# Performance work log

Measured on AMD Instinct MI355X. Metric: run time of the kernel, lower is better.

Reference implementation:

```python
import jax, jax.numpy as jnp
import numpy as np

B, T, F_IN = 256, 168, 128
H = 512            # encoder hidden per direction; decoder hidden = 2H
OUT = 1
L_OUT = 48
SCALE = 0.05


def _lstm_scan(x, Wih, Whh, b, h0, c0):
    # x: [T, B, F]; PyTorch LSTM gate order i, f, g, o
    def step(carry, xt):
        h, c = carry
        g = xt @ Wih.T + h @ Whh.T + b
        i, f, gg, o = jnp.split(g, 4, axis=-1)
        c = jax.nn.sigmoid(f) * c + jax.nn.sigmoid(i) * jnp.tanh(gg)
        h = jax.nn.sigmoid(o) * jnp.tanh(c)
        return (h, c), h
    (hT, cT), ys = jax.lax.scan(step, (h0, c0), x)
    return ys, hT, cT


def setup_inputs() -> dict:
    key = jax.random.key(0)
    ks = jax.random.split(key, 16)
    r = lambda k, shp: (jax.random.normal(k, shp, dtype=jnp.float32) * SCALE)
    return {
        "input_seq": jax.random.normal(ks[0], (B, T, F_IN), dtype=jnp.float32),
        "enc_Wih_f": r(ks[1], (4 * H, F_IN)),
        "enc_Whh_f": r(ks[2], (4 * H, H)),
        "enc_bih_f": r(ks[3], (4 * H,)),
        "enc_bhh_f": r(ks[4], (4 * H,)),
        "enc_Wih_b": r(ks[5], (4 * H, F_IN)),
        "enc_Whh_b": r(ks[6], (4 * H, H)),
        "enc_bih_b": r(ks[7], (4 * H,)),
        "enc_bhh_b": r(ks[8], (4 * H,)),
        "dec_Wih": r(ks[9], (4 * 2 * H, OUT)),
        "dec_Whh": r(ks[10], (4 * 2 * H, 2 * H)),
        "dec_bih": r(ks[11], (4 * 2 * H,)),
        "dec_bhh": r(ks[12], (4 * 2 * H,)),
        "fc_W": r(ks[13], (OUT, 2 * H)),
        "fc_b": r(ks[14], (OUT,)),
        "output_length": L_OUT,
    }


def reference(input_seq, enc_Wih_f, enc_Whh_f, enc_bih_f, enc_bhh_f,
              enc_Wih_b, enc_Whh_b, enc_bih_b, enc_bhh_b,
              dec_Wih, dec_Whh, dec_bih, dec_bhh, fc_W, fc_b, output_length):
    b = input_seq.shape[0]
    h = enc_Whh_f.shape[1]
    x = jnp.transpose(input_seq, (1, 0, 2))  # [T, B, F]
    h0 = jnp.zeros((b, h), input_seq.dtype)
    c0 = jnp.zeros((b, h), input_seq.dtype)
    # bidirectional encoder (final hidden/cell only are used downstream)
    _, hf, cf = _lstm_scan(x, enc_Wih_f, enc_Whh_f, enc_bih_f + enc_bhh_f, h0, c0)
    _, hb, cb = _lstm_scan(x[::-1], enc_Wih_b, enc_Whh_b, enc_bih_b + enc_bhh_b, h0, c0)
    # _cat_hidden: concat fwd/bwd states along feature dim -> decoder init state [B, 2H]
    hd = jnp.concatenate([hf, hb], axis=-1)
    cd = jnp.concatenate([cf, cb], axis=-1)
    bd = dec_bih + dec_bhh
    x0 = jnp.zeros((b, fc_W.shape[0]), input_seq.dtype)  # initial decoder input = zeros

    def dec_step(carry, _):
        hh, cc, xt = carry
        g = xt @ dec_Wih.T + hh @ dec_Whh.T + bd
        i, f, gg, o = jnp.split(g, 4, axis=-1)
        cc = jax.nn.sigmoid(f) * cc + jax.nn.sigmoid(i) * jnp.tanh(gg)
        hh = jax.nn.sigmoid(o) * jnp.tanh(cc)
        pred = hh @ fc_W.T + fc_b  # [B, OUT]
        return (hh, cc, pred), pred

    _, preds = jax.lax.scan(dec_step, (hd, cd, x0), None, length=output_length)
    # [L, B, OUT] -> [B, L, OUT] -> squeeze(dim=2) with OUT==1 -> [B, L]
    return jnp.transpose(preds, (1, 0, 2)).squeeze(2)
```

## Files before the change

kernel.cpp:

```cpp
#include <hip/hip_runtime.h>


constexpr int B_ = 256, T_ = 168, F_ = 128, H_ = 512, L_ = 48;
constexpr int KE = F_ + H_;
constexpr int HD = 1024;
constexpr int GE = 4 * H_;
constexpr int XPAD = 136;
constexpr int DPAD = HD + 8;

constexpr int FL256_IDX  = 0;
constexpr int CLAIM_IDX  = 256;
constexpr int ENCF_IDX   = 768;
constexpr int DECF_IDX   = 2816;
constexpr int CLAIM2_IDX = 3328;
constexpr int FL2_IDX    = 3840;

constexpr size_t OFF_SYNC = 0;
constexpr size_t OFF_WCF = 16384;
constexpr size_t OFF_WCB = OFF_WCF + (size_t)GE * KE * 2;
constexpr size_t OFF_PP  = OFF_WCB + (size_t)GE * KE * 2;
constexpr size_t OFF_BF  = OFF_PP  + (size_t)8 * 2 * 64 * 32 * 4;
constexpr size_t OFF_BB  = OFF_BF  + (size_t)GE * 4;
constexpr size_t OFF_XH  = OFF_BB  + (size_t)GE * 4;
constexpr size_t OFF_HE  = OFF_XH  + (size_t)T_ * B_ * F_ * 2;
constexpr size_t OFF_HDD = OFF_HE  + (size_t)2 * 2 * B_ * H_ * 2;
constexpr size_t OFF_CD  = OFF_HDD + (size_t)2 * B_ * HD * 2;

using h8 = __attribute__((ext_vector_type(8))) _Float16;
using f4 = __attribute__((ext_vector_type(4))) float;
using u4 = __attribute__((ext_vector_type(4))) unsigned;

#define DEV static __device__ __forceinline__

DEV float sigm(float x)  { return __fdividef(1.f, 1.f + __expf(-x)); }
DEV float tanh_(float x) { return 1.f - __fdividef(2.f, __expf(2.f * x) + 1.f); }

DEV h8 as_h8(f4 v) { union { f4 f; h8 h; } u; u.f = v; return u.h; }

DEV void astore_u64(void* p, unsigned long long v) {
  __hip_atomic_store((unsigned long long*)p, v, __ATOMIC_RELAXED,
                     __HIP_MEMORY_SCOPE_AGENT);
}
DEV void astore_u32(void* p, unsigned v) {
  __hip_atomic_store((unsigned*)p, v, __ATOMIC_RELAXED, __HIP_MEMORY_SCOPE_AGENT);
}
DEV unsigned aload_u32(const void* p) {
  return __hip_atomic_load((const unsigned*)p, __ATOMIC_RELAXED,
                           __HIP_MEMORY_SCOPE_AGENT);
}
DEV float aload_f32(const void* p) {
  return __hip_atomic_load((const float*)p, __ATOMIC_RELAXED,
                           __HIP_MEMORY_SCOPE_AGENT);
}
DEV void astore_f32(void* p, float v) {
  __hip_atomic_store((float*)p, v, __ATOMIC_RELAXED, __HIP_MEMORY_SCOPE_AGENT);
}
DEV void astore_u16(void* p, _Float16 v) {
  union { _Float16 h; unsigned short s; } u; u.h = v;
  __hip_atomic_store((unsigned short*)p, u.s, __ATOMIC_RELAXED,
                     __HIP_MEMORY_SCOPE_AGENT);
}
DEV void vm_drain() { asm volatile("s_waitcnt vmcnt(0)" ::: "memory"); }

template<bool DEEP>
DEV void ld16(const _Float16* p, f4* A) {
#define L16(FL) asm volatile( \
    "global_load_dwordx4 %0,  %16, off" FL "\n\t" \
    "global_load_dwordx4 %1,  %16, off offset:64" FL "\n\t" \
    "global_load_dwordx4 %2,  %16, off offset:128" FL "\n\t" \
    "global_load_dwordx4 %3,  %16, off offset:192" FL "\n\t" \
    "global_load_dwordx4 %4,  %16, off offset:256" FL "\n\t" \
    "global_load_dwordx4 %5,  %16, off offset:320" FL "\n\t" \
    "global_load_dwordx4 %6,  %16, off offset:384" FL "\n\t" \
    "global_load_dwordx4 %7,  %16, off offset:448" FL "\n\t" \
    "global_load_dwordx4 %8,  %16, off offset:512" FL "\n\t" \
    "global_load_dwordx4 %9,  %16, off offset:576" FL "\n\t" \
    "global_load_dwordx4 %10, %16, off offset:640" FL "\n\t" \
    "global_load_dwordx4 %11, %16, off offset:704" FL "\n\t" \
    "global_load_dwordx4 %12, %16, off offset:768" FL "\n\t" \
    "global_load_dwordx4 %13, %16, off offset:832" FL "\n\t" \
    "global_load_dwordx4 %14, %16, off offset:896" FL "\n\t" \
    "global_load_dwordx4 %15, %16, off offset:960" FL "\n\t" \
    "s_waitcnt vmcnt(0)" \
    : "=&v"(A[0]),"=&v"(A[1]),"=&v"(A[2]),"=&v"(A[3]),"=&v"(A[4]),"=&v"(A[5]), \
      "=&v"(A[6]),"=&v"(A[7]),"=&v"(A[8]),"=&v"(A[9]),"=&v"(A[10]),"=&v"(A[11]), \
      "=&v"(A[12]),"=&v"(A[13]),"=&v"(A[14]),"=&v"(A[15]) \
    : "v"(p) : "memory")
  if constexpr (DEEP) { L16(" sc0 sc1"); } else { L16(" sc0"); }
#undef L16
}

template<bool DEEP>
DEV void ld32(const _Float16* p, f4* A) {
#define L32(FL) asm volatile( \
    "global_load_dwordx4 %0,  %32, off" FL "\n\t" \
    "global_load_dwordx4 %1,  %32, off offset:64" FL "\n\t" \
    "global_load_dwordx4 %2,  %32, off offset:128" FL "\n\t" \
    "global_load_dwordx4 %3,  %32, off offset:192" FL "\n\t" \
    "global_load_dwordx4 %4,  %32, off offset:256" FL "\n\t" \
    "global_load_dwordx4 %5,  %32, off offset:320" FL "\n\t" \
    "global_load_dwordx4 %6,  %32, off offset:384" FL "\n\t" \
    "global_load_dwordx4 %7,  %32, off offset:448" FL "\n\t" \
    "global_load_dwordx4 %8,  %32, off offset:512" FL "\n\t" \
    "global_load_dwordx4 %9,  %32, off offset:576" FL "\n\t" \
    "global_load_dwordx4 %10, %32, off offset:640" FL "\n\t" \
    "global_load_dwordx4 %11, %32, off offset:704" FL "\n\t" \
    "global_load_dwordx4 %12, %32, off offset:768" FL "\n\t" \
    "global_load_dwordx4 %13, %32, off offset:832" FL "\n\t" \
    "global_load_dwordx4 %14, %32, off offset:896" FL "\n\t" \
    "global_load_dwordx4 %15, %32, off offset:960" FL "\n\t" \
    "global_load_dwordx4 %16, %32, off offset:1024" FL "\n\t" \
    "global_load_dwordx4 %17, %32, off offset:1088" FL "\n\t" \
    "global_load_dwordx4 %18, %32, off offset:1152" FL "\n\t" \
    "global_load_dwordx4 %19, %32, off offset:1216" FL "\n\t" \
    "global_load_dwordx4 %20, %32, off offset:1280" FL "\n\t" \
    "global_load_dwordx4 %21, %32, off offset:1344" FL "\n\t" \
    "global_load_dwordx4 %22, %32, off offset:1408" FL "\n\t" \
    "global_load_dwordx4 %23, %32, off offset:1472" FL "\n\t" \
    "global_load_dwordx4 %24, %32, off offset:1536" FL "\n\t" \
    "global_load_dwordx4 %25, %32, off offset:1600" FL "\n\t" \
    "global_load_dwordx4 %26, %32, off offset:1664" FL "\n\t" \
    "global_load_dwordx4 %27, %32, off offset:1728" FL "\n\t" \
    "global_load_dwordx4 %28, %32, off offset:1792" FL "\n\t" \
    "global_load_dwordx4 %29, %32, off offset:1856" FL "\n\t" \
    "global_load_dwordx4 %30, %32, off offset:1920" FL "\n\t" \
    "global_load_dwordx4 %31, %32, off offset:1984" FL "\n\t" \
    "s_waitcnt vmcnt(0)" \
    : "=&v"(A[0]),"=&v"(A[1]),"=&v"(A[2]),"=&v"(A[3]),"=&v"(A[4]),"=&v"(A[5]), \
      "=&v"(A[6]),"=&v"(A[7]),"=&v"(A[8]),"=&v"(A[9]),"=&v"(A[10]),"=&v"(A[11]), \
      "=&v"(A[12]),"=&v"(A[13]),"=&v"(A[14]),"=&v"(A[15]),"=&v"(A[16]),"=&v"(A[17]), \
      "=&v"(A[18]),"=&v"(A[19]),"=&v"(A[20]),"=&v"(A[21]),"=&v"(A[22]),"=&v"(A[23]), \
      "=&v"(A[24]),"=&v"(A[25]),"=&v"(A[26]),"=&v"(A[27]),"=&v"(A[28]),"=&v"(A[29]), \
      "=&v"(A[30]),"=&v"(A[31]) \
    : "v"(p) : "memory")
  if constexpr (DEEP) { L32(" sc0 sc1"); } else { L32(" sc0"); }
#undef L32
}

DEV void ld32s(const float* p, float* v) {
  asm volatile(
    "global_load_dword %0,  %32, off sc0 sc1\n\t"
    "global_load_dword %1,  %32, off offset:128 sc0 sc1\n\t"
    "global_load_dword %2,  %32, off offset:256 sc0 sc1\n\t"
    "global_load_dword %3,  %32, off offset:384 sc0 sc1\n\t"
    "global_load_dword %4,  %32, off offset:512 sc0 sc1\n\t"
    "global_load_dword %5,  %32, off offset:640 sc0 sc1\n\t"
    "global_load_dword %6,  %32, off offset:768 sc0 sc1\n\t"
    "global_load_dword %7,  %32, off offset:896 sc0 sc1\n\t"
    "global_load_dword %8,  %32, off offset:1024 sc0 sc1\n\t"
    "global_load_dword %9,  %32, off offset:1152 sc0 sc1\n\t"
    "global_load_dword %10, %32, off offset:1280 sc0 sc1\n\t"
    "global_load_dword %11, %32, off offset:1408 sc0 sc1\n\t"
    "global_load_dword %12, %32, off offset:1536 sc0 sc1\n\t"
    "global_load_dword %13, %32, off offset:1664 sc0 sc1\n\t"
    "global_load_dword %14, %32, off offset:1792 sc0 sc1\n\t"
    "global_load_dword %15, %32, off offset:1920 sc0 sc1\n\t"
    "global_load_dword %16, %32, off offset:2048 sc0 sc1\n\t"
    "global_load_dword %17, %32, off offset:2176 sc0 sc1\n\t"
    "global_load_dword %18, %32, off offset:2304 sc0 sc1\n\t"
    "global_load_dword %19, %32, off offset:2432 sc0 sc1\n\t"
    "global_load_dword %20, %32, off offset:2560 sc0 sc1\n\t"
    "global_load_dword %21, %32, off offset:2688 sc0 sc1\n\t"
    "global_load_dword %22, %32, off offset:2816 sc0 sc1\n\t"
    "global_load_dword %23, %32, off offset:2944 sc0 sc1\n\t"
    "global_load_dword %24, %32, off offset:3072 sc0 sc1\n\t"
    "global_load_dword %25, %32, off offset:3200 sc0 sc1\n\t"
    "global_load_dword %26, %32, off offset:3328 sc0 sc1\n\t"
    "global_load_dword %27, %32, off offset:3456 sc0 sc1\n\t"
    "global_load_dword %28, %32, off offset:3584 sc0 sc1\n\t"
    "global_load_dword %29, %32, off offset:3712 sc0 sc1\n\t"
    "global_load_dword %30, %32, off offset:3840 sc0 sc1\n\t"
    "global_load_dword %31, %32, off offset:3968 sc0 sc1\n\t"
    "s_waitcnt vmcnt(0)"
    : "=&v"(v[0]),"=&v"(v[1]),"=&v"(v[2]),"=&v"(v[3]),"=&v"(v[4]),"=&v"(v[5]),
      "=&v"(v[6]),"=&v"(v[7]),"=&v"(v[8]),"=&v"(v[9]),"=&v"(v[10]),"=&v"(v[11]),
      "=&v"(v[12]),"=&v"(v[13]),"=&v"(v[14]),"=&v"(v[15]),"=&v"(v[16]),"=&v"(v[17]),
      "=&v"(v[18]),"=&v"(v[19]),"=&v"(v[20]),"=&v"(v[21]),"=&v"(v[22]),"=&v"(v[23]),
      "=&v"(v[24]),"=&v"(v[25]),"=&v"(v[26]),"=&v"(v[27]),"=&v"(v[28]),"=&v"(v[29]),
      "=&v"(v[30]),"=&v"(v[31])
    : "v"(p) : "memory");
}

DEV unsigned pollflag(const unsigned* p, bool deep) {
  unsigned v;
  if (deep)
    asm volatile("global_load_dword %0, %1, off sc0 sc1\n\t"
                 "s_waitcnt vmcnt(0)" : "=&v"(v) : "v"(p) : "memory");
  else
    asm volatile("global_load_dword %0, %1, off sc0\n\t"
                 "s_waitcnt vmcnt(0)" : "=&v"(v) : "v"(p) : "memory");
  return v;
}
DEV void wait_ge(const unsigned* p, unsigned target, bool deep, int cap) {
  for (int it = 0; it < cap; ++it) {
    unsigned v = pollflag(p, deep);
    if (__ballot(v >= target) == ~0ull) return;
  }
}

DEV void gsync(unsigned* fl, int bi, unsigned phase, int tid) {
  vm_drain();
  __syncthreads();
  if (tid == 0) astore_u32(fl + bi, phase);
  if (tid < 64) {
    const unsigned* p = fl + tid * 4;
    for (int it = 0; it < (1 << 20); ++it) {
      u4 v;
      asm volatile("global_load_dwordx4 %0, %1, off sc0 sc1\n\t"
                   "s_waitcnt vmcnt(0)" : "=&v"(v) : "v"(p) : "memory");
      unsigned a = v[0] < v[1] ? v[0] : v[1];
      unsigned b = v[2] < v[3] ? v[2] : v[3];
      if (__ballot((a < b ? a : b) >= phase) == ~0ull) break;
    }
  }
  __syncthreads();
  asm volatile("" ::: "memory");
}

__global__ void prep_misc(const float* bihF, const float* bhhF,
                          const float* bihB, const float* bhhB, char* ws) {
  int i = blockIdx.x * blockDim.x + threadIdx.x;
  if (i < 2048) astore_u64(ws + (size_t)i * 8, 0ull);
  if (i < GE) {
    ((float*)(ws + OFF_BF))[i] = bihF[i] + bhhF[i];
    ((float*)(ws + OFF_BB))[i] = bihB[i] + bhhB[i];
  }
  if (i < 2 * 2 * B_ * H_ / 4) astore_u64((char*)ws + OFF_HE + (size_t)i * 8, 0ull);
}

__global__ void conv_encw(const float* WihF, const float* WhhF,
                          const float* WihB, const float* WhhB, char* ws) {
  int i = blockIdx.x * blockDim.x + threadIdx.x;
  if (i >= GE * KE) return;
  int r = i / KE, k = i - r * KE;
  float vF = (k < F_) ? WihF[r * F_ + k] : WhhF[r * H_ + (k - F_)];
  float vB = (k < F_) ? WihB[r * F_ + k] : WhhB[r * H_ + (k - F_)];
  ((_Float16*)(ws + OFF_WCF))[i] = (_Float16)vF;
  ((_Float16*)(ws + OFF_WCB))[i] = (_Float16)vB;
}

__global__ void conv_x(const float* x, char* ws) {
  int i = blockIdx.x * blockDim.x + threadIdx.x;
  if (i >= T_ * B_ * F_) return;
  int f = i & 127, b = (i >> 7) & 255, t = i >> 15;
  ((_Float16*)(ws + OFF_XH))[i] = (_Float16)x[((size_t)b * T_ + t) * F_ + f];
}

template<bool LOCAL>
DEV void encoder_phase(int dir, int chunk, int slice,
                       int tid, int wave, int quad, int col, int lane,
                       char* ws, _Float16* xlds, _Float16 (*htile)[64]) {
  const _Float16* Wenc  = (const _Float16*)(ws + (dir ? OFF_WCB : OFF_WCF));
  const float*    biasE = (const float*)(ws + (dir ? OFF_BB : OFF_BF));
  const _Float16* Xh    = (const _Float16*)(ws + OFF_XH);
  _Float16* hE = (_Float16*)(ws + OFF_HE);
  _Float16* hD = (_Float16*)(ws + OFF_HDD);
  float*    cD = (float*)(ws + OFF_CD);
  unsigned* encf = (unsigned*)ws + ENCF_IDX + (dir * 16 + chunk) * 64;

  const int j0 = slice * 64;
  const int mb = chunk * 16;

  for (int it = 0; it < 16; ++it) {
    int idx = it * 256 + tid;
    int n = idx >> 4, e = idx & 15;
    int g = n >> 6, u = n & 63;
    *((h8*)(xlds + (size_t)n * XPAD) + e) =
        *((const h8*)(Wenc + (size_t)(g * H_ + j0 + u) * KE) + e);
  }
  const int unit = j0 + wave * 16 + col;
  h8 Bf[4][16];
#pragma unroll
  for (int g = 0; g < 4; ++g)
#pragma unroll
    for (int kk = 0; kk < 16; ++kk)
      Bf[g][kk] = *((const h8*)(Wenc + (size_t)(g * H_ + unit) * KE + F_) +
                    kk * 4 + quad);
  float breg[4];
#pragma unroll
  for (int g = 0; g < 4; ++g) breg[g] = biasE[g * H_ + unit];
  float cst[4] = {0.f, 0.f, 0.f, 0.f};
  __syncthreads();

  const int arow  = mb + col;
  const int mrowq = mb + quad * 4;

  for (int t = 0; t < T_; ++t) {
    const int par = t & 1;
    const int tx  = dir ? (T_ - 1 - t) : t;
    f4 z = {0.f, 0.f, 0.f, 0.f};
    f4 acc[4] = {z, z, z, z};

    const h8* xr = (const h8*)(Xh + ((size_t)tx * B_ + arow) * F_);
#pragma unroll
    for (int kk = 0; kk < 4; ++kk) {
      h8 a = xr[kk * 4 + quad];
#pragma unroll
      for (int g = 0; g < 4; ++g) {
        h8 b = *((const h8*)(xlds + (size_t)(g * 64 + wave * 16 + col) * XPAD) +
                 kk * 4 + quad);
        acc[g] = __builtin_amdgcn_mfma_f32_16x16x32_f16(a, b, acc[g], 0, 0, 0);
      }
    }
    if (t > 0)
      wait_ge(encf + (lane & 7), (unsigned)t, !LOCAL, 1 << 16);
    f4 A[16];
    ld16<!LOCAL>(hE + ((size_t)(par * 2 + dir) * B_ + arow) * H_ + quad * 8, A);
#pragma unroll
    for (int kk = 0; kk < 16; ++kk) {
      h8 a = as_h8(A[kk]);
#pragma unroll
      for (int g = 0; g < 4; ++g)
        acc[g] = __builtin_amdgcn_mfma_f32_16x16x32_f16(a, Bf[g][kk], acc[g], 0, 0, 0);
    }

#pragma unroll
    for (int r = 0; r < 4; ++r) {
      float gi = acc[0][r] + breg[0];
      float gf = acc[1][r] + breg[1];
      float gg = acc[2][r] + breg[2];
      float go = acc[3][r] + breg[3];
      float c = sigm(gf) * cst[r] + sigm(gi) * tanh_(gg);
      cst[r] = c;
      float h = sigm(go) * tanh_(c);
      htile[quad * 4 + r][wave * 16 + col] = (_Float16)h;
      if (t == T_ - 1)
        astore_f32(&cD[(size_t)(mrowq + r) * HD + dir * H_ + unit], c);
    }
    __syncthreads();
    if (tid < 128) {
      int row = tid >> 3, seg = tid & 7;
      const unsigned long long* src =
          (const unsigned long long*)&htile[row][seg * 8];
      if (t < T_ - 1) {
        _Float16* dst = hE + ((size_t)((par ^ 1) * 2 + dir) * B_ + mb + row) * H_ +
                        j0 + seg * 8;
        if (LOCAL) {
          ((unsigned long long*)dst)[0] = src[0];
          ((unsigned long long*)(dst + 4))[0] = src[1];
        } else {
          astore_u64(dst, src[0]);
          astore_u64(dst + 4, src[1]);
        }
      } else {
        _Float16* dst = hD + (size_t)(mb + row) * HD + dir * H_ + j0 + seg * 8;
        astore_u64(dst, src[0]);
        astore_u64(dst + 4, src[1]);
      }
    }
    vm_drain();
    __syncthreads();
    if (tid == 0 && t < T_ - 1) {
      if (LOCAL) *(volatile unsigned*)(encf + slice) = (unsigned)(t + 1);
      else       astore_u32(encf + slice, (unsigned)(t + 1));
    }
  }
}

DEV void decoder_phase(int xcd, int rank, int tid, int wave, int quad, int col,
                       int lane, const float* dWih, const float* dWhh,
                       const float* dbih, const float* dbhh, const float* fcW,
                       const float* fcb, float* out, char* ws, _Float16* lds,
                       float* predbuf) {
  _Float16* hdd = (_Float16*)(ws + OFF_HDD);
  float* cD = (float*)(ws + OFF_CD);
  float* PP = (float*)(ws + OFF_PP) + (size_t)xcd * 2 * 64 * 32;
  unsigned* decf = (unsigned*)ws + DECF_IDX + xcd * 64;

  const int j0b = rank * 32;
  const int R0  = xcd * 32;
  const int m   = wave & 1;
  const int uh  = wave >> 1;
  const int unit = j0b + uh * 16 + col;
  const int arow = R0 + m * 16 + col;
  const int mrow = R0 + m * 16 + quad * 4;

  for (int it = 0; it < 64; ++it) {
    int idx = it * 256 + tid;
    int n = idx >> 8, c = idx & 255;
    int srow = (n >> 5) * HD + j0b + (n & 31);
    f4 w = *((const f4*)(dWhh + (size_t)srow * HD + c * 4));
    union { _Float16 h[4]; unsigned long long q; } u2;
#pragma unroll
    for (int i2 = 0; i2 < 4; ++i2) u2.h[i2] = (_Float16)w[i2];
    *(unsigned long long*)(lds + n * DPAD + c * 4) = u2.q;
  }
  h8 Bf[2][32];
#pragma unroll
  for (int gg = 0; gg < 2; ++gg)
#pragma unroll
    for (int kk = 0; kk < 32; ++kk) {
      const float* src = dWhh + (size_t)((2 + gg) * HD + unit) * HD + kk * 32 + quad * 8;
      f4 w0 = *((const f4*)src);
      f4 w1 = *((const f4*)(src + 4));
      union { _Float16 h[8]; h8 v; } u3;
#pragma unroll
      for (int i2 = 0; i2 < 4; ++i2) {
        u3.h[i2]     = (_Float16)w0[i2];
        u3.h[4 + i2] = (_Float16)w1[i2];
      }
      Bf[gg][kk] = u3.v;
    }
  float breg[4], wreg[4];
#pragma unroll
  for (int g = 0; g < 4; ++g) {
    breg[g] = dbih[g * HD + unit] + dbhh[g * HD + unit];
    wreg[g] = dWih[g * HD + unit];
  }
  const float fcw = fcW[unit];
  const float fb  = fcb[0];
  float cst[4];
#pragma unroll
  for (int r = 0; r < 4; ++r)
    cst[r] = aload_f32(cD + (size_t)(mrow + r) * HD + unit);
  __syncthreads();

  for (int l = 0; l <= L_; ++l) {
    float predv = 0.f;
    if (l > 0) {
      wait_ge(decf + (lane & 31), (unsigned)l, true, 1 << 16);
      const float* PPr = PP + (size_t)((l - 1) & 1) * 64 * 32;
      int row = lane & 31, halfsel = lane >> 5;
      const float* pb = PPr + (size_t)(halfsel * 32) * 32 + row;
      float pv[32], s = 0.f;
      ld32s(pb, pv);
#pragma unroll
      for (int j = 0; j < 32; ++j) s += pv[j];
      s += __shfl_xor(s, 32);
      predv = s + fb;
      if (rank == 0 && wave == 0 && lane < 32)
        predbuf[(l - 1) * 32 + lane] = predv;
    }
    if (l == L_) break;
    const int par = l & 1;

    f4 A[32];
    ld32<true>(hdd + ((size_t)par * B_ + arow) * HD + quad * 8, A);

    f4 z = {0.f, 0.f, 0.f, 0.f};
    f4 acc[4] = {z, z, z, z};
#pragma unroll
    for (int kk = 0; kk < 32; ++kk) {
      h8 a = as_h8(A[kk]);
      h8 b0 = *((const h8*)(lds + (0 * 32 + uh * 16 + col) * DPAD) + kk * 4 + quad);
      h8 b1 = *((const h8*)(lds + (1 * 32 + uh * 16 + col) * DPAD) + kk * 4 + quad);
      acc[0] = __builtin_amdgcn_mfma_f32_16x16x32_f16(a, b0, acc[0], 0, 0, 0);
      acc[1] = __builtin_amdgcn_mfma_f32_16x16x32_f16(a, b1, acc[1], 0, 0, 0);
      acc[2] = __builtin_amdgcn_mfma_f32_16x16x32_f16(a, Bf[0][kk], acc[2], 0, 0, 0);
      acc[3] = __builtin_amdgcn_mfma_f32_16x16x32_f16(a, Bf[1][kk], acc[3], 0, 0, 0);
    }

    float pr[4], sum[4];
#pragma unroll
    for (int r = 0; r < 4; ++r)
      pr[r] = (l > 0) ? __shfl(predv, m * 16 + quad * 4 + r) : 0.f;
#pragma unroll
    for (int r = 0; r < 4; ++r) {
      float gi = acc[0][r] + breg[0] + pr[r] * wreg[0];
      float gf = acc[1][r] + breg[1] + pr[r] * wreg[1];
      float gg = acc[2][r] + breg[2] + pr[r] * wreg[2];
      float go = acc[3][r] + breg[3] + pr[r] * wreg[3];
      float c = sigm(gf) * cst[r] + sigm(gi) * tanh_(gg);
      cst[r] = c;
      float h = sigm(go) * tanh_(c);
      size_t hoff = ((size_t)(par ^ 1) * B_ + mrow + r) * HD + unit;
      astore_u16(hdd + hoff, (_Float16)h);
      sum[r] = h * fcw;
    }
#pragma unroll
    for (int off = 1; off < 16; off <<= 1) {
#pragma unroll
      for (int r = 0; r < 4; ++r) sum[r] += __shfl_xor(sum[r], off, 16);
    }
    if (col == 0) {
      float* PPw = PP + (size_t)(l & 1) * 64 * 32;
      float* pdst = PPw + (size_t)(rank * 2 + uh) * 32 + m * 16 + quad * 4;
      union { float f[4]; unsigned long long q[2]; } u5;
#pragma unroll
      for (int r = 0; r < 4; ++r) u5.f[r] = sum[r];
      astore_u64(pdst, u5.q[0]);
      astore_u64(pdst + 2, u5.q[1]);
    }
    vm_drain();
    __syncthreads();
    if (tid == 0) astore_u32(decf + rank, (unsigned)(l + 1));
  }

  if (rank == 0) {
    __syncthreads();
    for (int idx = tid; idx < L_ * 32; idx += 256) {
      int row2 = idx & 31, st = idx >> 5;
      out[(size_t)(R0 + row2) * L_ + st] = predbuf[st * 32 + row2];
    }
  }
}

__global__ __launch_bounds__(256, 1)
void enc_kernel(char* __restrict__ ws) {
  __shared__ __align__(16) _Float16 xlds[256 * XPAD];
  __shared__ __align__(16) _Float16 htile[16][64];
  __shared__ int sh[2];

  const int tid  = threadIdx.x;
  const int wave = tid >> 6;
  const int lane = tid & 63;
  const int quad = lane >> 4;
  const int col  = lane & 15;
  const int bi   = blockIdx.x;

  unsigned* sync  = (unsigned*)(ws + OFF_SYNC);
  unsigned* fl    = sync + FL256_IDX;
  unsigned* claim = sync + CLAIM_IDX;

  if (tid == 0) {
    unsigned x;
    asm volatile("s_getreg_b32 %0, hwreg(HW_REG_XCC_ID)" : "=s"(x));
    int xcd = (int)(x & 7u);
    unsigned r = __hip_atomic_fetch_add(claim + xcd * 64, 1u, __ATOMIC_RELAXED,
                                        __HIP_MEMORY_SCOPE_AGENT);
    sh[0] = xcd;
    sh[1] = (int)r;
  }
  __syncthreads();
  const int xcd = sh[0], rank = sh[1];
  gsync(fl, bi, 1u, tid);
  if (tid == 0) {
    int d = 0;
    for (int k = 0; k < 8; ++k)
      if (aload_u32(claim + k * 64) != 32u) d = 1;
    sh[0] = d;
  }
  __syncthreads();
  const bool deg = (sh[0] != 0) || (rank >= 32);

  if (!deg) {
    encoder_phase<true>(xcd >> 2, (xcd & 3) * 4 + (rank >> 3), rank & 7,
                        tid, wave, quad, col, lane, ws, xlds, htile);
  } else {
    int d2 = bi >> 7, rest = bi & 127;
    encoder_phase<false>(d2, rest >> 3, rest & 7,
                         tid, wave, quad, col, lane, ws, xlds, htile);
  }
}

__global__ __launch_bounds__(256, 1)
void dec_kernel(const float* __restrict__ dWih, const float* __restrict__ dWhh,
                const float* __restrict__ dbih, const float* __restrict__ dbhh,
                const float* __restrict__ fcW, const float* __restrict__ fcb,
                float* __restrict__ out, char* __restrict__ ws) {
  __shared__ __align__(16) _Float16 lds[64 * DPAD];
  __shared__ __align__(16) float predbuf[L_ * 32];
  __shared__ int sh[2];

  const int tid  = threadIdx.x;
  const int wave = tid >> 6;
  const int lane = tid & 63;
  const int quad = lane >> 4;
  const int col  = lane & 15;
  const int bi   = blockIdx.x;

  unsigned* sync  = (unsigned*)(ws + OFF_SYNC);
  unsigned* fl2   = sync + FL2_IDX;
  unsigned* claim = sync + CLAIM2_IDX;

  if (tid == 0) {
    unsigned x;
    asm volatile("s_getreg_b32 %0, hwreg(HW_REG_XCC_ID)" : "=s"(x));
    int xcd = (int)(x & 7u);
    unsigned r = __hip_atomic_fetch_add(claim + xcd * 64, 1u, __ATOMIC_RELAXED,
                                        __HIP_MEMORY_SCOPE_AGENT);
    sh[0] = xcd;
    sh[1] = (int)r;
  }
  __syncthreads();
  const int xcd = sh[0], rank = sh[1];
  gsync(fl2, bi, 1u, tid);
  if (tid == 0) {
    int d = 0;
    for (int k = 0; k < 8; ++k)
      if (aload_u32(claim + k * 64) != 32u) d = 1;
    sh[0] = d;
  }
  __syncthreads();
  const bool deg = (sh[0] != 0) || (rank >= 32);

  if (!deg)
    decoder_phase(xcd, rank, tid, wave, quad, col, lane, dWih, dWhh,
                  dbih, dbhh, fcW, fcb, out, ws, lds, predbuf);
  else
    decoder_phase(bi >> 5, bi & 31, tid, wave, quad, col, lane, dWih,
                  dWhh, dbih, dbhh, fcW, fcb, out, ws, lds, predbuf);
}

extern "C" void kernel_launch(void* const* d_in, const int* in_sizes, int n_in,
                              void* d_out, int out_size, void* d_ws, size_t ws_size,
                              hipStream_t stream) {
  const float* x     = (const float*)d_in[0];
  const float* eWihF = (const float*)d_in[1];
  const float* eWhhF = (const float*)d_in[2];
  const float* ebihF = (const float*)d_in[3];
  const float* ebhhF = (const float*)d_in[4];
  const float* eWihB = (const float*)d_in[5];
  const float* eWhhB = (const float*)d_in[6];
  const float* ebihB = (const float*)d_in[7];
  const float* ebhhB = (const float*)d_in[8];
  const float* dWih  = (const float*)d_in[9];
  const float* dWhh  = (const float*)d_in[10];
  const float* dbih  = (const float*)d_in[11];
  const float* dbhh  = (const float*)d_in[12];
  const float* fcW   = (const float*)d_in[13];
  const float* fcb   = (const float*)d_in[14];
  float* out = (float*)d_out;
  char*  ws  = (char*)d_ws;

  prep_misc<<<512, 256, 0, stream>>>(ebihF, ebhhF, ebihB, ebhhB, ws);
  conv_encw<<<(GE * KE) / 256, 256, 0, stream>>>(eWihF, eWhhF, eWihB, eWhhB, ws);
  conv_x<<<(T_ * B_ * F_) / 256, 256, 0, stream>>>(x, ws);

  enc_kernel<<<dim3(256), dim3(256), 0, stream>>>(ws);
  dec_kernel<<<dim3(256), dim3(256), 0, stream>>>(dWih, dWhh, dbih, dbhh,
                                                  fcW, fcb, out, ws);
}
```

Measured before the change: 1.415 ms.

## Fuse encoder flag polling with hidden-state load and prefetch next x tile

The encoder step now issues the readiness-flag load and the 16 hidden-state vector loads in one batch. It retries the whole batch until every lane sees the flag, which removes a serial poll-then-load round trip from each recurrent step. The input tile for the next timestep is now loaded into registers before the end-of-step drain, instead of being loaded at the start of the next step. The risk is that the data loads are not ordered after the flag load, so a stale hidden state could be consumed. Failed polls also now re-read the full hidden-state rows, which adds memory traffic.

```diff
diff --git a/kernel.cpp b/kernel.cpp
--- a/kernel.cpp
+++ b/kernel.cpp
@@ -88,6 +88,36 @@
     : "v"(p) : "memory")
   if constexpr (DEEP) { L16(" sc0 sc1"); } else { L16(" sc0"); }
 #undef L16
+}
+
+template<bool DEEP>
+DEV void ldwait16(const unsigned* pf, const _Float16* p, f4* A, unsigned* fv) {
+#define LW16(FL) asm volatile( \
+    "global_load_dword %0, %17, off" FL "\n\t" \
+    "global_load_dwordx4 %1,  %18, off" FL "\n\t" \
+    "global_load_dwordx4 %2,  %18, off offset:64" FL "\n\t" \
+    "global_load_dwordx4 %3,  %18, off offset:128" FL "\n\t" \
+    "global_load_dwordx4 %4,  %18, off offset:192" FL "\n\t" \
+    "global_load_dwordx4 %5,  %18, off offset:256" FL "\n\t" \
+    "global_load_dwordx4 %6,  %18, off offset:320" FL "\n\t" \
+    "global_load_dwordx4 %7,  %18, off offset:384" FL "\n\t" \
+    "global_load_dwordx4 %8,  %18, off offset:448" FL "\n\t" \
+    "global_load_dwordx4 %9,  %18, off offset:512" FL "\n\t" \
+    "global_load_dwordx4 %10, %18, off offset:576" FL "\n\t" \
+    "global_load_dwordx4 %11, %18, off offset:640" FL "\n\t" \
+    "global_load_dwordx4 %12, %18, off offset:704" FL "\n\t" \
+    "global_load_dwordx4 %13, %18, off offset:768" FL "\n\t" \
+    "global_load_dwordx4 %14, %18, off offset:832" FL "\n\t" \
+    "global_load_dwordx4 %15, %18, off offset:896" FL "\n\t" \
+    "global_load_dwordx4 %16, %18, off offset:960" FL "\n\t" \
+    "s_waitcnt vmcnt(0)" \
+    : "=&v"(*fv), \
+      "=&v"(A[0]),"=&v"(A[1]),"=&v"(A[2]),"=&v"(A[3]),"=&v"(A[4]),"=&v"(A[5]), \
+      "=&v"(A[6]),"=&v"(A[7]),"=&v"(A[8]),"=&v"(A[9]),"=&v"(A[10]),"=&v"(A[11]), \
+      "=&v"(A[12]),"=&v"(A[13]),"=&v"(A[14]),"=&v"(A[15]) \
+    : "v"(pf), "v"(p) : "memory")
+  if constexpr (DEEP) { LW16(" sc0 sc1"); } else { LW16(" sc0"); }
+#undef LW16
 }
 
 template<bool DEEP>
@@ -285,27 +315,41 @@
   const int arow  = mb + col;
   const int mrowq = mb + quad * 4;
 
+  h8 xa[4];
+  {
+    const int tx0 = dir ? (T_ - 1) : 0;
+    const h8* xr = (const h8*)(Xh + ((size_t)tx0 * B_ + arow) * F_);
+#pragma unroll
+    for (int kk = 0; kk < 4; ++kk) xa[kk] = xr[kk * 4 + quad];
+  }
+
   for (int t = 0; t < T_; ++t) {
     const int par = t & 1;
-    const int tx  = dir ? (T_ - 1 - t) : t;
     f4 z = {0.f, 0.f, 0.f, 0.f};
     f4 acc[4] = {z, z, z, z};
 
-    const h8* xr = (const h8*)(Xh + ((size_t)tx * B_ + arow) * F_);
 #pragma unroll
     for (int kk = 0; kk < 4; ++kk) {
-      h8 a = xr[kk * 4 + quad];
 #pragma unroll
       for (int g = 0; g < 4; ++g) {
         h8 b = *((const h8*)(xlds + (size_t)(g * 64 + wave * 16 + col) * XPAD) +
                  kk * 4 + quad);
-        acc[g] = __builtin_amdgcn_mfma_f32_16x16x32_f16(a, b, acc[g], 0, 0, 0);
+        acc[g] = __builtin_amdgcn_mfma_f32_16x16x32_f16(xa[kk], b, acc[g], 0, 0, 0);
       }
     }
-    if (t > 0)
-      wait_ge(encf + (lane & 7), (unsigned)t, !LOCAL, 1 << 16);
+
     f4 A[16];
-    ld16<!LOCAL>(hE + ((size_t)(par * 2 + dir) * B_ + arow) * H_ + quad * 8, A);
+    const _Float16* hptr =
+        hE + ((size_t)(par * 2 + dir) * B_ + arow) * H_ + quad * 8;
+    if (t > 0) {
+      unsigned fv;
+      for (int it2 = 0; it2 < (1 << 16); ++it2) {
+        ldwait16<!LOCAL>(encf + (lane & 7), hptr, A, &fv);
+        if (__ballot(fv >= (unsigned)t) == ~0ull) break;
+      }
+    } else {
+      ld16<!LOCAL>(hptr, A);
+    }
 #pragma unroll
     for (int kk = 0; kk < 16; ++kk) {
       h8 a = as_h8(A[kk]);
@@ -348,6 +392,12 @@
         astore_u64(dst + 4, src[1]);
       }
     }
+    if (t < T_ - 1) {
+      const int txn = dir ? (T_ - 2 - t) : (t + 1);
+      const h8* xr = (const h8*)(Xh + ((size_t)txn * B_ + arow) * F_);
+#pragma unroll
+      for (int kk = 0; kk < 4; ++kk) xa[kk] = xr[kk * 4 + quad];
+    }
     vm_drain();
     __syncthreads();
     if (tid == 0 && t < T_ - 1) {
```

After: 1.403 ms. No clear change (-0.9%).
